# Kernel tuning notes

Measured on AMD Instinct MI355X. Metric: run time of the kernel, lower is better.

The kernel has to match this reference:

```python
import jax, jax.numpy as jnp
import numpy as np

B, C_IN, T, C_OUT, K = 32, 1024, 512, 1024, 3


def conv1d(x, w, b, stride, pad):
    # x: (B, Cin, L), w: (Cout, Cin, K)
    y = jax.lax.conv_general_dilated(
        x, w, window_strides=(stride,), padding=[(pad, pad)],
        dimension_numbers=("NCH", "OIH", "NCH"))
    return y + b[None, :, None]


def setup_inputs() -> dict:
    key = jax.random.key(0)
    k1, k2, k3, k4, k5 = jax.random.split(key, 5)
    inputs = jax.random.normal(k1, (B, C_IN, T), dtype=jnp.float32)
    # offset conv is zero-initialized in the module; use small random values
    # so the deformable path is actually exercised.
    w_off = jax.random.normal(k2, (K, C_IN, K), dtype=jnp.float32) * 0.01
    b_off = jax.random.normal(k3, (K,), dtype=jnp.float32) * 0.01
    w_conv = jax.random.normal(k4, (C_OUT, C_IN, K), dtype=jnp.float32) * (1.0 / np.sqrt(C_IN * K))
    b_conv = jax.random.normal(k5, (C_OUT,), dtype=jnp.float32) * 0.01
    return {"inputs": inputs, "w_off": w_off, "b_off": b_off,
            "w_conv": w_conv, "b_conv": b_conv}


def _forward(inputs, w_off, b_off, w_conv, b_conv):
    Bb, C, Tt = inputs.shape
    Kk = w_off.shape[0]
    half = Kk // 2
    H, W = Tt, C  # grid_sample view: (B, 1, H=T, W=C)

    # offset prediction conv (stride 1, padding K//2) -> (B, K, T) -> (B, T, K)
    offsets = conv1d(inputs, w_off, b_off, 1, half)
    pred = jnp.transpose(offsets, (0, 2, 1))  # (B, H, K)

    # normalized y grid (align_corners=True style normalization, as in _make_grid)
    pos = jnp.arange(-half, half + 1, dtype=jnp.float32)  # (K,)
    base = (jnp.arange(H, dtype=jnp.float32) / (H - 1)) * 2.0 - 1.0  # (H,)
    g = base[None, :, None] + pos[None, None, :] * (2.0 / (H - 1)) + pred  # (B,H,K)
    g = jnp.clip(g, -1.0, 1.0)

    # F.grid_sample default align_corners=False: pixel = ((g+1)*size - 1)/2
    py = ((g + 1.0) * H - 1.0) * 0.5  # (B, H, K)
    y0 = jnp.floor(py)
    ty = py - y0
    y0i = y0.astype(jnp.int32)
    y0c = jnp.clip(y0i, 0, H - 1)      # border padding
    y1c = jnp.clip(y0i + 1, 0, H - 1)

    # x grid is data-independent: w_grid = w/(W-1)*2-1, so pixel_x = w*W/(W-1)-0.5
    wj = jnp.arange(W, dtype=jnp.float32)
    px = wj * (W / (W - 1.0)) - 0.5
    x0 = jnp.floor(px)
    tx = px - x0
    x0i = x0.astype(jnp.int32)
    x0c = jnp.clip(x0i, 0, W - 1)
    x1c = jnp.clip(x0i + 1, 0, W - 1)

    A = jnp.transpose(inputs, (0, 2, 1))  # (B, H, W)
    # separable bilinear: mix along W first (offset only shifts y)
    xmix = (1.0 - tx)[None, None, :] * A[:, :, x0c] + tx[None, None, :] * A[:, :, x1c]  # (B,H,W)

    b_ix = jnp.arange(Bb)[:, None, None]
    g0 = xmix[b_ix, y0c]  # (B, H, K, W)
    g1 = xmix[b_ix, y1c]  # (B, H, K, W)
    sampled = (1.0 - ty)[..., None] * g0 + ty[..., None] * g1  # (B, H, K, W)

    # final conv over kernel axis: (B*H, W=C_in, K) -> (B, H, C_out)
    out = jnp.einsum("bhkw,owk->bho", sampled, w_conv) + b_conv[None, None, :]
    return out


def reference(inputs, w_off, b_off, w_conv, b_conv):
    return _forward(inputs, w_off, b_off, w_conv, b_conv)
```

## Files before the change

kernel.cpp:

```cpp
#include <hip/hip_runtime.h>

#define NB 32
#define NC 1024
#define NT 512
#define NO 1024
#define KTILES 48

typedef __attribute__((ext_vector_type(8))) short bf16x8;
typedef __attribute__((ext_vector_type(4))) float f32x4;

#define FENCE asm volatile("" ::: "memory")
#define BAR do{ FENCE; __builtin_amdgcn_s_barrier(); FENCE; }while(0)
#define LGKM0 asm volatile("s_waitcnt lgkmcnt(0)" ::: "memory")

__device__ __forceinline__ unsigned short f2bf(float f){
  unsigned int i = __float_as_uint(f);
  i += 0x7fffu + ((i >> 16) & 1u);
  return (unsigned short)(i >> 16);
}

__device__ __forceinline__ unsigned int blend_pack(unsigned int u0, unsigned int u1, float t){
  float a0 = __uint_as_float(u0 << 16);
  float a1 = __uint_as_float(u0 & 0xffff0000u);
  float b0 = __uint_as_float(u1 << 16);
  float b1 = __uint_as_float(u1 & 0xffff0000u);
  float r0 = fmaf(t, b0 - a0, a0);
  float r1 = fmaf(t, b1 - a1, a1);
  return (unsigned int)f2bf(r0) | (((unsigned int)f2bf(r1)) << 16);
}

__device__ __forceinline__ void async16(const void* g, void* l){
  __builtin_amdgcn_global_load_lds((const __attribute__((address_space(1))) void*)g,
                                   (__attribute__((address_space(3))) void*)l, 16, 0, 0);
}

__global__ __launch_bounds__(256) void transpose_off_kernel(const float* __restrict__ x,
    const float* __restrict__ w_off, unsigned short* __restrict__ atr,
    float* __restrict__ part){
  __shared__ float tile[64][67];
  __shared__ float wsh[64][9];
  __shared__ float red[4][64][3];
  int b = blockIdx.z, c0 = blockIdx.y * 64, t0 = blockIdx.x * 64;
  int tx = threadIdx.x & 63, wy = threadIdx.x >> 6;
  const float* xp = x + ((size_t)b * NC + c0) * NT + t0;
  #pragma unroll
  for (int i = 0; i < 16; i++){ int cl = wy * 16 + i; tile[cl][1 + tx] = xp[(size_t)cl * NT + tx]; }
  if (threadIdx.x < 64){
    tile[tx][0]  = (t0 > 0)       ? xp[(size_t)tx * NT - 1]  : 0.f;
  } else if (threadIdx.x < 128){
    tile[tx][65] = (t0 + 64 < NT) ? xp[(size_t)tx * NT + 64] : 0.f;
  }
  for (int i = threadIdx.x; i < 576; i += 256){
    int c = i / 9, r = i % 9;
    wsh[c][r] = w_off[(size_t)(r / 3) * 3072 + (size_t)(c0 + c) * 3 + (r % 3)];
  }
  __syncthreads();
  int p = threadIdx.x & 31, r2 = threadIdx.x >> 5;
  unsigned int* dst = (unsigned int*)(atr + ((size_t)b * NT + t0) * NC + c0);
  #pragma unroll
  for (int i = 0; i < 8; i++){
    int tl = r2 * 8 + i;
    unsigned int lo = f2bf(tile[2 * p][1 + tl]);
    unsigned int hi = f2bf(tile[2 * p + 1][1 + tl]);
    dst[(size_t)tl * (NC / 2) + p] = lo | (hi << 16);
  }
  float s0 = 0.f, s1 = 0.f, s2 = 0.f;
  #pragma unroll 4
  for (int i = 0; i < 16; i++){
    int c = wy * 16 + i;
    float xm = tile[c][tx], xc = tile[c][1 + tx], xq = tile[c][2 + tx];
    s0 += xm * wsh[c][0] + xc * wsh[c][1] + xq * wsh[c][2];
    s1 += xm * wsh[c][3] + xc * wsh[c][4] + xq * wsh[c][5];
    s2 += xm * wsh[c][6] + xc * wsh[c][7] + xq * wsh[c][8];
  }
  red[wy][tx][0] = s0; red[wy][tx][1] = s1; red[wy][tx][2] = s2;
  __syncthreads();
  if (threadIdx.x < 192){
    int tl = threadIdx.x & 63, o = threadIdx.x >> 6;
    float v = red[0][tl][o] + red[1][tl][o] + red[2][tl][o] + red[3][tl][o];
    size_t m = (size_t)b * NT + t0 + tl;
    part[(m * 3 + o) * 16 + blockIdx.y] = v;
  }
}

__global__ __launch_bounds__(256) void index_kernel(const float* __restrict__ part,
    const float* __restrict__ b_off, int* __restrict__ i0a, int* __restrict__ i1a,
    float* __restrict__ tya){
  int gid = blockIdx.x * 256 + threadIdx.x;
  int o = gid % 3, m = gid / 3, tt = m & 511;
  const float* pp = part + (size_t)gid * 16;
  float p = b_off[o];
  #pragma unroll
  for (int i = 0; i < 16; i++) p += pp[i];
  float base = (float)tt / 511.0f * 2.0f - 1.0f;
  float g = base + (float)(o - 1) * (float)(2.0 / 511.0) + p;
  g = fminf(1.0f, fmaxf(-1.0f, g));
  float py = ((g + 1.0f) * 512.0f - 1.0f) * 0.5f;
  float y0 = floorf(py);
  int i0 = (int)y0;
  i0a[gid] = min(max(i0, 0), NT - 1);
  i1a[gid] = min(max(i0 + 1, 0), NT - 1);
  tya[gid] = py - y0;
}

__global__ __launch_bounds__(256) void wmix_kernel(const float* __restrict__ w_conv,
                                                   unsigned short* __restrict__ wm2){
  int gid = blockIdx.x * 256 + threadIdx.x;
  int o = gid >> 10, c = gid & 1023;
  const float ratio = (float)(1024.0 / 1023.0);
  float acc0 = 0.f, acc1 = 0.f, acc2 = 0.f;
  int wlo = (c > 2) ? c - 2 : 0;
  int whi = (c < 1021) ? c + 2 : 1023;
  for (int w = wlo; w <= whi; ++w){
    float px = (float)w * ratio - 0.5f;
    float x0 = floorf(px);
    float tx = px - x0;
    int i0 = (int)x0;
    int i0c = min(max(i0, 0), 1023);
    int i1c = min(max(i0 + 1, 0), 1023);
    float s = ((i0c == c) ? (1.0f - tx) : 0.f) + ((i1c == c) ? tx : 0.f);
    if (s != 0.f){
      const float* wc = w_conv + ((size_t)o * 1024 + w) * 3;
      acc0 += s * wc[0]; acc1 += s * wc[1]; acc2 += s * wc[2];
    }
  }
  size_t base = (size_t)o * 3072 + c;
  wm2[base]        = f2bf(acc0);
  wm2[base + 1024] = f2bf(acc1);
  wm2[base + 2048] = f2bf(acc2);
}

__global__ __launch_bounds__(256) void blend_kernel(
    const unsigned short* __restrict__ atr, const int* __restrict__ i0a,
    const int* __restrict__ i1a, const float* __restrict__ tya,
    unsigned short* __restrict__ Abl){
  int k = blockIdx.y;
  int row = blockIdx.x * 2 + (threadIdx.x >> 7);
  int seg = threadIdx.x & 127;
  int idx = row * 3 + k;
  int b = row >> 9;
  const unsigned short* base = atr + (size_t)b * NT * NC;
  const uint4* r0 = (const uint4*)(base + (size_t)i0a[idx] * NC);
  const uint4* r1 = (const uint4*)(base + (size_t)i1a[idx] * NC);
  float t = tya[idx];
  uint4 v0 = r0[seg], v1 = r1[seg], rv;
  rv.x = blend_pack(v0.x, v1.x, t);
  rv.y = blend_pack(v0.y, v1.y, t);
  rv.z = blend_pack(v0.z, v1.z, t);
  rv.w = blend_pack(v0.w, v1.w, t);
  *(uint4*)(Abl + (size_t)row * 3072 + (size_t)k * 1024 + (size_t)seg * 8) = rv;
}

__device__ __forceinline__ void stage_half(const unsigned short* __restrict__ src,
                                           unsigned short* Lbase, int row0, int q,
                                           int w, int lane){
  int l3 = lane >> 3, l7 = lane & 7;
  int swc = ((l7 ^ l3) << 3);
  #pragma unroll
  for (int i = 0; i < 2; i++){
    int ci = i * 8 + w;
    const unsigned short* g = src + (size_t)(row0 + ci * 8 + l3) * 3072 + q * 64 + swc;
    async16(g, Lbase + ci * 512);
  }
}

__global__ __launch_bounds__(512, 2) void gemm8_kernel(
    const unsigned short* __restrict__ A, const unsigned short* __restrict__ Bw,
    const float* __restrict__ b_conv, float* __restrict__ out){
  __shared__ __align__(16) unsigned short L[65536];

  int wg = blockIdx.x;
  int swz = (wg & 7) * 32 + (wg >> 3);
  int mtile = swz >> 2, ntile = swz & 3;
  int m0 = mtile * 256, n0 = ntile * 256;
  int tid = threadIdx.x, lane = tid & 63, w = tid >> 6;
  int wm_ = w >> 2, wn_ = w & 3;
  int lq = lane & 15, q4 = lane >> 4;
  int sl0 = (q4 ^ (lq & 7)) << 3;
  int sl1 = ((4 + q4) ^ (lq & 7)) << 3;
  int hb = wn_ >> 1, nb = (wn_ & 1) * 64;

  f32x4 acc[8][4];
  #pragma unroll
  for (int i = 0; i < 8; i++)
    #pragma unroll
    for (int j = 0; j < 4; j++) acc[i][j] = (f32x4){0.f, 0.f, 0.f, 0.f};

  stage_half(A,  &L[0],                 m0,       0, w, lane);
  stage_half(A,  &L[8192],              m0 + 128, 0, w, lane);
  stage_half(Bw, &L[16384],             n0,       0, w, lane);
  stage_half(Bw, &L[16384 + 8192],      n0 + 128, 0, w, lane);
  stage_half(Bw, &L[32768 + 16384],        n0,       1, w, lane);
  stage_half(Bw, &L[32768 + 16384 + 8192], n0 + 128, 1, w, lane);
  asm volatile("s_waitcnt vmcnt(4)" ::: "memory");
  BAR;

  bf16x8 aA[4][2], bB[4][2];

  for (int t = 0; t < KTILES; ++t){
    int c = (t & 1) * 32768;
    int cn = ((t + 1) & 1) * 32768;
    const unsigned short* LA = &L[c + wm_ * 8192];
    const unsigned short* LB = &L[c + 16384 + hb * 8192];

    #pragma unroll
    for (int mf = 0; mf < 4; mf++){
      int r = mf * 16 + lq;
      aA[mf][0] = *(const bf16x8*)&LA[r * 64 + sl0];
      aA[mf][1] = *(const bf16x8*)&LA[r * 64 + sl1];
    }
    #pragma unroll
    for (int nf = 0; nf < 2; nf++){
      int r = nb + nf * 16 + lq;
      bB[nf][0] = *(const bf16x8*)&LB[r * 64 + sl0];
      bB[nf][1] = *(const bf16x8*)&LB[r * 64 + sl1];
    }
    if (t + 1 < KTILES) stage_half(A, &L[cn], m0, t + 1, w, lane);
    BAR; LGKM0;
    __builtin_amdgcn_s_setprio(1);
    #pragma unroll
    for (int mf = 0; mf < 4; mf++)
      #pragma unroll
      for (int nf = 0; nf < 2; nf++){
        acc[mf][nf] = __builtin_amdgcn_mfma_f32_16x16x32_bf16(aA[mf][0], bB[nf][0], acc[mf][nf], 0, 0, 0);
        acc[mf][nf] = __builtin_amdgcn_mfma_f32_16x16x32_bf16(aA[mf][1], bB[nf][1], acc[mf][nf], 0, 0, 0);
      }
    __builtin_amdgcn_s_setprio(0);
    BAR;

    #pragma unroll
    for (int nf = 2; nf < 4; nf++){
      int r = nb + nf * 16 + lq;
      bB[nf][0] = *(const bf16x8*)&LB[r * 64 + sl0];
      bB[nf][1] = *(const bf16x8*)&LB[r * 64 + sl1];
    }
    if (t + 1 < KTILES) stage_half(A, &L[cn + 8192], m0 + 128, t + 1, w, lane);
    BAR; LGKM0;
    __builtin_amdgcn_s_setprio(1);
    #pragma unroll
    for (int mf = 0; mf < 4; mf++)
      #pragma unroll
      for (int nf = 2; nf < 4; nf++){
        acc[mf][nf] = __builtin_amdgcn_mfma_f32_16x16x32_bf16(aA[mf][0], bB[nf][0], acc[mf][nf], 0, 0, 0);
        acc[mf][nf] = __builtin_amdgcn_mfma_f32_16x16x32_bf16(aA[mf][1], bB[nf][1], acc[mf][nf], 0, 0, 0);
      }
    __builtin_amdgcn_s_setprio(0);
    BAR;

    #pragma unroll
    for (int mf = 0; mf < 4; mf++){
      int r = 64 + mf * 16 + lq;
      aA[mf][0] = *(const bf16x8*)&LA[r * 64 + sl0];
      aA[mf][1] = *(const bf16x8*)&LA[r * 64 + sl1];
    }
    if (t + 2 < KTILES) stage_half(Bw, &L[c + 16384], n0, t + 2, w, lane);
    BAR; LGKM0;
    __builtin_amdgcn_s_setprio(1);
    #pragma unroll
    for (int mf = 0; mf < 4; mf++)
      #pragma unroll
      for (int nf = 2; nf < 4; nf++){
        acc[4 + mf][nf] = __builtin_amdgcn_mfma_f32_16x16x32_bf16(aA[mf][0], bB[nf][0], acc[4 + mf][nf], 0, 0, 0);
        acc[4 + mf][nf] = __builtin_amdgcn_mfma_f32_16x16x32_bf16(aA[mf][1], bB[nf][1], acc[4 + mf][nf], 0, 0, 0);
      }
    __builtin_amdgcn_s_setprio(0);
    BAR;

    if (t + 2 < KTILES) stage_half(Bw, &L[c + 16384 + 8192], n0 + 128, t + 2, w, lane);
    BAR;
    __builtin_amdgcn_s_setprio(1);
    #pragma unroll
    for (int mf = 0; mf < 4; mf++)
      #pragma unroll
      for (int nf = 0; nf < 2; nf++){
        acc[4 + mf][nf] = __builtin_amdgcn_mfma_f32_16x16x32_bf16(aA[mf][0], bB[nf][0], acc[4 + mf][nf], 0, 0, 0);
        acc[4 + mf][nf] = __builtin_amdgcn_mfma_f32_16x16x32_bf16(aA[mf][1], bB[nf][1], acc[4 + mf][nf], 0, 0, 0);
      }
    __builtin_amdgcn_s_setprio(0);
    if (t + 2 < KTILES)      { asm volatile("s_waitcnt vmcnt(4)" ::: "memory"); }
    else if (t + 1 < KTILES) { asm volatile("s_waitcnt vmcnt(0)" ::: "memory"); }
    BAR;
  }

  #pragma unroll
  for (int nf = 0; nf < 4; nf++){
    int n = n0 + wn_ * 64 + nf * 16 + lq;
    float bc = b_conv[n];
    #pragma unroll
    for (int mh = 0; mh < 2; mh++)
      #pragma unroll
      for (int mf = 0; mf < 4; mf++){
        int mr = m0 + wm_ * 128 + mh * 64 + mf * 16 + q4 * 4;
        f32x4 v = acc[mh * 4 + mf][nf];
        #pragma unroll
        for (int j = 0; j < 4; j++)
          out[(size_t)(mr + j) * NO + n] = v[j] + bc;
      }
  }
}

extern "C" void kernel_launch(void* const* d_in, const int* in_sizes, int n_in,
                              void* d_out, int out_size, void* d_ws, size_t ws_size,
                              hipStream_t stream){
  (void)in_sizes; (void)n_in; (void)out_size; (void)ws_size;
  const float* x      = (const float*)d_in[0];
  const float* w_off  = (const float*)d_in[1];
  const float* b_off  = (const float*)d_in[2];
  const float* w_conv = (const float*)d_in[3];
  const float* b_conv = (const float*)d_in[4];
  float* out = (float*)d_out;

  char* ws = (char*)d_ws;
  unsigned short* atr = (unsigned short*)ws;
  float* part = (float*)(ws + 33554432);
  int*   i0a  = (int*)  (ws + 33554432 + 3145728);
  int*   i1a  = (int*)  (ws + 33554432 + 3145728 + 196608);
  float* tya  = (float*)(ws + 33554432 + 3145728 + 393216);
  unsigned short* wm2 = (unsigned short*)(ws + 37289984);
  unsigned short* Abl = (unsigned short*)(ws + 43581440);

  hipLaunchKernelGGL(transpose_off_kernel, dim3(NT / 64, NC / 64, NB), dim3(256), 0, stream,
                     x, w_off, atr, part);
  hipLaunchKernelGGL(index_kernel, dim3(49152 / 256), dim3(256), 0, stream,
                     part, b_off, i0a, i1a, tya);
  hipLaunchKernelGGL(wmix_kernel,  dim3((1024 * 1024) / 256), dim3(256), 0, stream, w_conv, wm2);
  hipLaunchKernelGGL(blend_kernel, dim3(16384 / 2, 3), dim3(256), 0, stream,
                     atr, i0a, i1a, tya, Abl);
  hipLaunchKernelGGL(gemm8_kernel, dim3((16384 / 256) * (1024 / 256)), dim3(512), 0, stream,
                     Abl, wm2, b_conv, out);
}
```

Baseline: 170.7 us.

## Restructure GEMM LDS fragment loads to prefetch next tile and merge blend launches

The GEMM main loop now keeps separate register sets for the first and second A halves and for both B halves. It loads the next tile's A-first-half and all B fragments at the end of each iteration, so fewer LDS reads sit on the critical path before the MFMAs, and the explicit lgkmcnt waits are dropped. The blend kernel now processes all three kernel taps in one thread, issuing six gathers up front and launching one grid dimension instead of three. The cost is higher register pressure under launch_bounds(512,2). It also relies on compiler-inserted waits for LDS reads to be correct.

```diff
diff --git a/kernel.cpp b/kernel.cpp
--- a/kernel.cpp
+++ b/kernel.cpp
@@ -11,7 +11,6 @@
 
 #define FENCE asm volatile("" ::: "memory")
 #define BAR do{ FENCE; __builtin_amdgcn_s_barrier(); FENCE; }while(0)
-#define LGKM0 asm volatile("s_waitcnt lgkmcnt(0)" ::: "memory")
 
 __device__ __forceinline__ unsigned short f2bf(float f){
   unsigned int i = __float_as_uint(f);
@@ -134,21 +133,28 @@
     const unsigned short* __restrict__ atr, const int* __restrict__ i0a,
     const int* __restrict__ i1a, const float* __restrict__ tya,
     unsigned short* __restrict__ Abl){
-  int k = blockIdx.y;
   int row = blockIdx.x * 2 + (threadIdx.x >> 7);
   int seg = threadIdx.x & 127;
-  int idx = row * 3 + k;
   int b = row >> 9;
   const unsigned short* base = atr + (size_t)b * NT * NC;
-  const uint4* r0 = (const uint4*)(base + (size_t)i0a[idx] * NC);
-  const uint4* r1 = (const uint4*)(base + (size_t)i1a[idx] * NC);
-  float t = tya[idx];
-  uint4 v0 = r0[seg], v1 = r1[seg], rv;
-  rv.x = blend_pack(v0.x, v1.x, t);
-  rv.y = blend_pack(v0.y, v1.y, t);
-  rv.z = blend_pack(v0.z, v1.z, t);
-  rv.w = blend_pack(v0.w, v1.w, t);
-  *(uint4*)(Abl + (size_t)row * 3072 + (size_t)k * 1024 + (size_t)seg * 8) = rv;
+  unsigned short* orow = Abl + (size_t)row * 3072 + (size_t)seg * 8;
+  uint4 v0[3], v1[3]; float t[3];
+  #pragma unroll
+  for (int k = 0; k < 3; k++){
+    int idx = row * 3 + k;
+    v0[k] = *(const uint4*)(base + (size_t)i0a[idx] * NC + (size_t)seg * 8);
+    v1[k] = *(const uint4*)(base + (size_t)i1a[idx] * NC + (size_t)seg * 8);
+    t[k] = tya[idx];
+  }
+  #pragma unroll
+  for (int k = 0; k < 3; k++){
+    uint4 rv;
+    rv.x = blend_pack(v0[k].x, v1[k].x, t[k]);
+    rv.y = blend_pack(v0[k].y, v1[k].y, t[k]);
+    rv.z = blend_pack(v0[k].z, v1[k].z, t[k]);
+    rv.w = blend_pack(v0[k].w, v1[k].w, t[k]);
+    *(uint4*)(orow + k * 1024) = rv;
+  }
 }
 
 __device__ __forceinline__ void stage_half(const unsigned short* __restrict__ src,
@@ -195,73 +201,74 @@
   asm volatile("s_waitcnt vmcnt(4)" ::: "memory");
   BAR;
 
-  bf16x8 aA[4][2], bB[4][2];
+  bf16x8 aC[4][2], aN[4][2], b01[2][2], b23[2][2];
+
+  {
+    const unsigned short* LA = &L[wm_ * 8192];
+    const unsigned short* LB = &L[16384 + hb * 8192];
+    #pragma unroll
+    for (int mf = 0; mf < 4; mf++){
+      int r = mf * 16 + lq;
+      aC[mf][0] = *(const bf16x8*)&LA[r * 64 + sl0];
+      aC[mf][1] = *(const bf16x8*)&LA[r * 64 + sl1];
+    }
+    #pragma unroll
+    for (int nf = 0; nf < 2; nf++){
+      int r = nb + nf * 16 + lq;
+      b01[nf][0] = *(const bf16x8*)&LB[r * 64 + sl0];
+      b01[nf][1] = *(const bf16x8*)&LB[r * 64 + sl1];
+      int r2 = nb + (nf + 2) * 16 + lq;
+      b23[nf][0] = *(const bf16x8*)&LB[r2 * 64 + sl0];
+      b23[nf][1] = *(const bf16x8*)&LB[r2 * 64 + sl1];
+    }
+  }
 
   for (int t = 0; t < KTILES; ++t){
     int c = (t & 1) * 32768;
     int cn = ((t + 1) & 1) * 32768;
     const unsigned short* LA = &L[c + wm_ * 8192];
-    const unsigned short* LB = &L[c + 16384 + hb * 8192];
-
-    #pragma unroll
-    for (int mf = 0; mf < 4; mf++){
-      int r = mf * 16 + lq;
-      aA[mf][0] = *(const bf16x8*)&LA[r * 64 + sl0];
-      aA[mf][1] = *(const bf16x8*)&LA[r * 64 + sl1];
-    }
-    #pragma unroll
-    for (int nf = 0; nf < 2; nf++){
-      int r = nb + nf * 16 + lq;
-      bB[nf][0] = *(const bf16x8*)&LB[r * 64 + sl0];
-      bB[nf][1] = *(const bf16x8*)&LB[r * 64 + sl1];
-    }
-    if (t + 1 < KTILES) stage_half(A, &L[cn], m0, t + 1, w, lane);
-    BAR; LGKM0;
-    __builtin_amdgcn_s_setprio(1);
-    #pragma unroll
-    for (int mf = 0; mf < 4; mf++)
-      #pragma unroll
-      for (int nf = 0; nf < 2; nf++){
-        acc[mf][nf] = __builtin_amdgcn_mfma_f32_16x16x32_bf16(aA[mf][0], bB[nf][0], acc[mf][nf], 0, 0, 0);
-        acc[mf][nf] = __builtin_amdgcn_mfma_f32_16x16x32_bf16(aA[mf][1], bB[nf][1], acc[mf][nf], 0, 0, 0);
-      }
-    __builtin_amdgcn_s_setprio(0);
-    BAR;
-
-    #pragma unroll
-    for (int nf = 2; nf < 4; nf++){
-      int r = nb + nf * 16 + lq;
-      bB[nf][0] = *(const bf16x8*)&LB[r * 64 + sl0];
-      bB[nf][1] = *(const bf16x8*)&LB[r * 64 + sl1];
-    }
-    if (t + 1 < KTILES) stage_half(A, &L[cn + 8192], m0 + 128, t + 1, w, lane);
-    BAR; LGKM0;
-    __builtin_amdgcn_s_setprio(1);
-    #pragma unroll
-    for (int mf = 0; mf < 4; mf++)
-      #pragma unroll
-      for (int nf = 2; nf < 4; nf++){
-        acc[mf][nf] = __builtin_amdgcn_mfma_f32_16x16x32_bf16(aA[mf][0], bB[nf][0], acc[mf][nf], 0, 0, 0);
-        acc[mf][nf] = __builtin_amdgcn_mfma_f32_16x16x32_bf16(aA[mf][1], bB[nf][1], acc[mf][nf], 0, 0, 0);
-      }
-    __builtin_amdgcn_s_setprio(0);
-    BAR;
 
     #pragma unroll
     for (int mf = 0; mf < 4; mf++){
       int r = 64 + mf * 16 + lq;
-      aA[mf][0] = *(const bf16x8*)&LA[r * 64 + sl0];
-      aA[mf][1] = *(const bf16x8*)&LA[r * 64 + sl1];
-    }
+      aN[mf][0] = *(const bf16x8*)&LA[r * 64 + sl0];
+      aN[mf][1] = *(const bf16x8*)&LA[r * 64 + sl1];
+    }
+    if (t + 1 < KTILES) stage_half(A, &L[cn], m0, t + 1, w, lane);
+    BAR;
+    __builtin_amdgcn_s_setprio(1);
+    #pragma unroll
+    for (int mf = 0; mf < 4; mf++)
+      #pragma unroll
+      for (int nf = 0; nf < 2; nf++){
+        acc[mf][nf] = __builtin_amdgcn_mfma_f32_16x16x32_bf16(aC[mf][0], b01[nf][0], acc[mf][nf], 0, 0, 0);
+        acc[mf][nf] = __builtin_amdgcn_mfma_f32_16x16x32_bf16(aC[mf][1], b01[nf][1], acc[mf][nf], 0, 0, 0);
+      }
+    __builtin_amdgcn_s_setprio(0);
+    BAR;
+
+    if (t + 1 < KTILES) stage_half(A, &L[cn + 8192], m0 + 128, t + 1, w, lane);
+    BAR;
+    __builtin_amdgcn_s_setprio(1);
+    #pragma unroll
+    for (int mf = 0; mf < 4; mf++)
+      #pragma unroll
+      for (int nf = 0; nf < 2; nf++){
+        acc[mf][2 + nf] = __builtin_amdgcn_mfma_f32_16x16x32_bf16(aC[mf][0], b23[nf][0], acc[mf][2 + nf], 0, 0, 0);
+        acc[mf][2 + nf] = __builtin_amdgcn_mfma_f32_16x16x32_bf16(aC[mf][1], b23[nf][1], acc[mf][2 + nf], 0, 0, 0);
+      }
+    __builtin_amdgcn_s_setprio(0);
+    BAR;
+
     if (t + 2 < KTILES) stage_half(Bw, &L[c + 16384], n0, t + 2, w, lane);
-    BAR; LGKM0;
+    BAR;
     __builtin_amdgcn_s_setprio(1);
     #pragma unroll
     for (int mf = 0; mf < 4; mf++)
       #pragma unroll
-      for (int nf = 2; nf < 4; nf++){
-        acc[4 + mf][nf] = __builtin_amdgcn_mfma_f32_16x16x32_bf16(aA[mf][0], bB[nf][0], acc[4 + mf][nf], 0, 0, 0);
-        acc[4 + mf][nf] = __builtin_amdgcn_mfma_f32_16x16x32_bf16(aA[mf][1], bB[nf][1], acc[4 + mf][nf], 0, 0, 0);
+      for (int nf = 0; nf < 2; nf++){
+        acc[4 + mf][2 + nf] = __builtin_amdgcn_mfma_f32_16x16x32_bf16(aN[mf][0], b23[nf][0], acc[4 + mf][2 + nf], 0, 0, 0);
+        acc[4 + mf][2 + nf] = __builtin_amdgcn_mfma_f32_16x16x32_bf16(aN[mf][1], b23[nf][1], acc[4 + mf][2 + nf], 0, 0, 0);
       }
     __builtin_amdgcn_s_setprio(0);
     BAR;
@@ -273,13 +280,33 @@
     for (int mf = 0; mf < 4; mf++)
       #pragma unroll
       for (int nf = 0; nf < 2; nf++){
-        acc[4 + mf][nf] = __builtin_amdgcn_mfma_f32_16x16x32_bf16(aA[mf][0], bB[nf][0], acc[4 + mf][nf], 0, 0, 0);
-        acc[4 + mf][nf] = __builtin_amdgcn_mfma_f32_16x16x32_bf16(aA[mf][1], bB[nf][1], acc[4 + mf][nf], 0, 0, 0);
+        acc[4 + mf][nf] = __builtin_amdgcn_mfma_f32_16x16x32_bf16(aN[mf][0], b01[nf][0], acc[4 + mf][nf], 0, 0, 0);
+        acc[4 + mf][nf] = __builtin_amdgcn_mfma_f32_16x16x32_bf16(aN[mf][1], b01[nf][1], acc[4 + mf][nf], 0, 0, 0);
       }
     __builtin_amdgcn_s_setprio(0);
     if (t + 2 < KTILES)      { asm volatile("s_waitcnt vmcnt(4)" ::: "memory"); }
     else if (t + 1 < KTILES) { asm volatile("s_waitcnt vmcnt(0)" ::: "memory"); }
     BAR;
+
+    if (t + 1 < KTILES){
+      const unsigned short* LAn = &L[cn + wm_ * 8192];
+      const unsigned short* LBn = &L[cn + 16384 + hb * 8192];
+      #pragma unroll
+      for (int mf = 0; mf < 4; mf++){
+        int r = mf * 16 + lq;
+        aC[mf][0] = *(const bf16x8*)&LAn[r * 64 + sl0];
+        aC[mf][1] = *(const bf16x8*)&LAn[r * 64 + sl1];
+      }
+      #pragma unroll
+      for (int nf = 0; nf < 2; nf++){
+        int r = nb + nf * 16 + lq;
+        b01[nf][0] = *(const bf16x8*)&LBn[r * 64 + sl0];
+        b01[nf][1] = *(const bf16x8*)&LBn[r * 64 + sl1];
+        int r2 = nb + (nf + 2) * 16 + lq;
+        b23[nf][0] = *(const bf16x8*)&LBn[r2 * 64 + sl0];
+        b23[nf][1] = *(const bf16x8*)&LBn[r2 * 64 + sl1];
+      }
+    }
   }
 
   #pragma unroll
@@ -324,7 +351,7 @@
   hipLaunchKernelGGL(index_kernel, dim3(49152 / 256), dim3(256), 0, stream,
                      part, b_off, i0a, i1a, tya);
   hipLaunchKernelGGL(wmix_kernel,  dim3((1024 * 1024) / 256), dim3(256), 0, stream, w_conv, wm2);
-  hipLaunchKernelGGL(blend_kernel, dim3(16384 / 2, 3), dim3(256), 0, stream,
+  hipLaunchKernelGGL(blend_kernel, dim3(16384 / 2), dim3(256), 0, stream,
                      atr, i0a, i1a, tya, Abl);
   hipLaunchKernelGGL(gemm8_kernel, dim3((16384 / 256) * (1024 / 256)), dim3(512), 0, stream,
                      Abl, wm2, b_conv, out);
```

Measured after the change: 170.6 us. No clear change (-0.1%).
